# Performance work log

Hardware: AMD Instinct MI355X
Metric: run time of the kernel (lower is better)

Reference implementation:

```python
import jax, jax.numpy as jnp
import numpy as np

N_DRUG = 846
E = 64          # embedding_num
S = 1024        # neighbor_sample_size
T_LEN = 50000   # tail entity vocab
R_LEN = 100     # relation vocab
BN_EPS = 1e-5


def setup_inputs() -> dict:
    key = jax.random.key(0)
    ks = jax.random.split(key, 12)
    inp = {
        'drug_name': jnp.arange(N_DRUG, dtype=jnp.int64) if jax.config.jax_enable_x64 else jnp.arange(N_DRUG, dtype=jnp.int32),
        'adj_tail': jax.random.randint(ks[0], (N_DRUG, S), 0, T_LEN),
        'adj_relation': jax.random.randint(ks[1], (N_DRUG, S), 0, R_LEN),
        # learned parameters
        'drug_table': jax.random.normal(ks[2], (N_DRUG, E), jnp.float32),
        'rela_table': jax.random.normal(ks[3], (R_LEN, E), jnp.float32),
        'ent_table': jax.random.normal(ks[4], (T_LEN, E), jnp.float32),
        'W1': jax.random.normal(ks[5], (N_DRUG, E, E), jnp.float32),
        'b1': jax.random.normal(ks[6], (S, E), jnp.float32),
        'W2': jax.random.normal(ks[7], (N_DRUG, E, E), jnp.float32),
        'b2': jax.random.normal(ks[8], (S, E), jnp.float32),
        'lin_W': jax.random.normal(ks[9], (E, 2 * E), jnp.float32) * (6.0 / (3 * E)) ** 0.5,  # xavier-ish
        'lin_b': jnp.zeros((E,), jnp.float32),
        'bn_gamma': jnp.ones((E,), jnp.float32),
        'bn_beta': jnp.zeros((E,), jnp.float32),
    }
    return inp


def _forward(drug_table, rela_table, ent_table, W1, b1, W2, b2,
             lin_W, lin_b, bn_gamma, bn_beta,
             drug_name, adj_tail, adj_relation):
    drug_emb = drug_table[drug_name]                     # [N, E]
    rela_emb = rela_table[adj_relation]                  # [N, S, E]
    ent_emb = ent_table[adj_tail]                        # [N, S, E]

    drug_rel = drug_emb[:, None, :] * rela_emb           # [N, S, E]
    h = jax.nn.relu(jnp.einsum('nse,nef->nsf', drug_rel, W1) + b1)
    h = jnp.einsum('nse,nef->nsf', h, W2) + b2           # [N, S, E]
    score = jnp.sum(h, axis=-1)                          # [N, S]
    attn = jax.nn.softmax(score, axis=1)                 # softmax over neighbors
    weighted_ent = jnp.einsum('ns,nse->ne', attn, ent_emb)  # [N, E]

    drug_e = jnp.concatenate([weighted_ent, drug_emb], axis=1)  # [N, 2E]
    x = jax.nn.relu(drug_e @ lin_W.T + lin_b)            # [N, E]
    # BatchNorm1d in training mode: biased batch stats over the node dim
    mean = jnp.mean(x, axis=0)
    var = jnp.var(x, axis=0)
    drug_f = (x - mean) * jax.lax.rsqrt(var + BN_EPS) * bn_gamma + bn_beta
    return drug_f


def reference(drug_name, adj_tail, adj_relation, drug_table, rela_table,
              ent_table, W1, b1, W2, b2, lin_W, lin_b, bn_gamma, bn_beta):
    return _forward(drug_table, rela_table, ent_table, W1, b1, W2, b2,
                    lin_W, lin_b, bn_gamma, bn_beta,
                    drug_name, adj_tail, adj_relation)
```

## Files before the change

### kernel.cpp

```cpp
#include <hip/hip_runtime.h>

#define NDRUG 846
#define EDIM  64
#define SNB   1024
#define RLEN  100

#define XBUF_OFF  0
#define B2SUM_OFF (NDRUG*EDIM)

__global__ __launch_bounds__(256) void prep2(const float* __restrict__ b2,
                                             float* __restrict__ b2sum)
{
  int t = threadIdx.x;
  int s = blockIdx.x*64 + (t >> 2);
  int q = t & 3;
  const float4* p = reinterpret_cast<const float4*>(b2 + (size_t)s*EDIM) + q*4;
  float4 a = p[0], b = p[1], c = p[2], d = p[3];
  float v = (a.x+a.y+a.z+a.w) + (b.x+b.y+b.z+b.w)
          + (c.x+c.y+c.z+c.w) + (d.x+d.y+d.z+d.w);
  v += __shfl_xor(v, 1);
  v += __shfl_xor(v, 2);
  if (q == 0) b2sum[s] = v;
}

__global__ __launch_bounds__(512, 4) void gnn_main(
    const int*   __restrict__ adj_tail,  const int* __restrict__ adj_relation,
    const float* __restrict__ drug_table, const float* __restrict__ rela_table,
    const float* __restrict__ ent_table, const float* __restrict__ W1,
    const float* __restrict__ W2,        const float* __restrict__ b1,
    const float* __restrict__ lin_W,     const float* __restrict__ lin_b,
    const float* __restrict__ b2sum,     float* __restrict__ xbuf)
{
  __shared__ __align__(16) float lds[13128];
  float* g_s     = lds;
  float* dr_s    = lds + 6600;
  float* w2sum_s = lds + 13000;
  float* demb_s  = lds + 13064;
  float* score_s = dr_s;
  unsigned long long* msk = reinterpret_cast<unsigned long long*>(dr_s + 1024);
  float* went_s  = g_s;
  float* red_s   = g_s + 64;
  float* mred    = g_s + 576;

  int n  = blockIdx.x;
  int t  = threadIdx.x;
  int w8 = __builtin_amdgcn_readfirstlane(t >> 6);
  int ln = t & 63;

  float w1c[64];
  {
    const float* w1p = W1 + (size_t)n*4096 + ln;
    #pragma unroll
    for (int e = 0; e < 64; ++e) w1c[e] = w1p[e*64];
  }

  {
    const float4* rel4 = reinterpret_cast<const float4*>(rela_table);
    const float4* dv4  = reinterpret_cast<const float4*>(drug_table + (size_t)n*EDIM);
    float4* drw = reinterpret_cast<float4*>(dr_s);
    for (int i = t; i < 1600; i += 512) {
      float4 rv = rel4[i];
      float4 dv = dv4[i & 15];
      float4 o;
      o.x = rv.x*dv.x; o.y = rv.y*dv.y; o.z = rv.z*dv.z; o.w = rv.w*dv.w;
      drw[i] = o;
    }
    const float4* w2p4 = reinterpret_cast<const float4*>(W2 + (size_t)n*4096);
    float4 a = w2p4[t*2], b = w2p4[t*2+1];
    float s8 = (a.x+a.y+a.z+a.w) + (b.x+b.y+b.z+b.w);
    s8 += __shfl_xor(s8, 1);
    s8 += __shfl_xor(s8, 2);
    s8 += __shfl_xor(s8, 4);
    if ((t & 7) == 0) w2sum_s[t >> 3] = s8;
    if (t < EDIM) demb_s[t] = drug_table[(size_t)n*EDIM + t];
  }
  __syncthreads();

  {
    int base = (w8 < 4) ? w8*13 : 52 + (w8-4)*12;
    int nr   = (w8 < 4) ? 13 : 12;
    for (int rr = 0; rr < nr; ++rr) {
      int r = base + rr;
      const float4* drr = reinterpret_cast<const float4*>(dr_s + r*64);
      float acc = 0.f;
      #pragma unroll
      for (int e4 = 0; e4 < 16; ++e4) {
        float4 d = drr[e4];
        acc = fmaf(d.x, w1c[e4*4+0], acc);
        acc = fmaf(d.y, w1c[e4*4+1], acc);
        acc = fmaf(d.z, w1c[e4*4+2], acc);
        acc = fmaf(d.w, w1c[e4*4+3], acc);
      }
      g_s[r*66 + ln] = acc;
    }
  }
  __syncthreads();

  {
    int fq = ln & 3;
    float w2r[16];
    #pragma unroll
    for (int jj = 0; jj < 4; ++jj) {
      float4 v4 = *reinterpret_cast<const float4*>(w2sum_s + jj*16 + fq*4);
      w2r[jj*4+0] = v4.x; w2r[jj*4+1] = v4.y; w2r[jj*4+2] = v4.z; w2r[jj*4+3] = v4.w;
    }
    for (int it = 0; it < 8; ++it) {
      int s   = it*128 + (t >> 2);
      int rel = adj_relation[(size_t)n*SNB + s];
      const float4* b1r = reinterpret_cast<const float4*>(b1 + (size_t)s*EDIM);
      const float2* g2  = reinterpret_cast<const float2*>(g_s + rel*66);
      float acc = 0.f;
      #pragma unroll
      for (int jj = 0; jj < 4; ++jj) {
        float4 bv = b1r[jj*4 + fq];
        int gi = jj*8 + fq*2;
        float2 ga = g2[gi], gb = g2[gi+1];
        float h0 = fmaxf(ga.x + bv.x, 0.f);
        float h1 = fmaxf(ga.y + bv.y, 0.f);
        float h2 = fmaxf(gb.x + bv.z, 0.f);
        float h3 = fmaxf(gb.y + bv.w, 0.f);
        acc = fmaf(h0, w2r[jj*4+0], acc);
        acc = fmaf(h1, w2r[jj*4+1], acc);
        acc = fmaf(h2, w2r[jj*4+2], acc);
        acc = fmaf(h3, w2r[jj*4+3], acc);
      }
      acc += __shfl_xor(acc, 1);
      acc += __shfl_xor(acc, 2);
      if (fq == 0) score_s[s] = acc + b2sum[s];
    }
  }
  __syncthreads();

  float av0, av1;
  {
    float s0 = score_s[t], s1 = score_s[512 + t];
    float m = fmaxf(s0, s1);
    #pragma unroll
    for (int o = 32; o >= 1; o >>= 1) m = fmaxf(m, __shfl_xor(m, o));
    if (ln == 0) mred[w8] = m;
    __syncthreads();
    float M = mred[0];
    #pragma unroll
    for (int k = 1; k < 8; ++k) M = fmaxf(M, mred[k]);
    float e0 = __expf(s0 - M), e1 = __expf(s1 - M);
    float sum = e0 + e1;
    #pragma unroll
    for (int o = 32; o >= 1; o >>= 1) sum += __shfl_xor(sum, o);
    if (ln == 0) mred[8 + w8] = sum;
    __syncthreads();
    float S = mred[8];
    #pragma unroll
    for (int k = 9; k < 16; ++k) S += mred[k];
    float inv = 1.0f / S;
    av0 = e0*inv; av1 = e1*inv;
    score_s[t] = av0;
    score_s[512 + t] = av1;
  }

  {
    unsigned long long m0 = __ballot(av0 > 2e-9f);
    unsigned long long m1 = __ballot(av1 > 2e-9f);
    if (ln == 0) { msk[w8] = m0; msk[8 + w8] = m1; }
  }
  __syncthreads();
  if (w8 == 0) {
    float acc = 0.f;
    const int* tails = adj_tail + (size_t)n*SNB;
    for (int c = 0; c < 16; ++c) {
      unsigned long long mm = msk[c];
      int sbase = (c < 8) ? c*64 : 512 + (c - 8)*64;
      while (mm) {
        int bpos = __ffsll((unsigned long long)mm) - 1;
        mm &= mm - 1;
        int s = sbase + bpos;
        float av = score_s[s];
        int tl = tails[s];
        acc = fmaf(av, ent_table[(size_t)tl*EDIM + ln], acc);
      }
    }
    went_s[ln] = acc;
  }
  __syncthreads();

  {
    float acc = 0.f;
    const float* lw = lin_W + (size_t)ln*128 + w8*16;
    #pragma unroll
    for (int k = 0; k < 16; ++k) {
      int kk = w8*16 + k;
      float cv = (kk < 64) ? went_s[kk] : demb_s[kk - 64];
      acc = fmaf(cv, lw[k], acc);
    }
    red_s[w8*64 + ln] = acc;
  }
  __syncthreads();
  if (t < EDIM) {
    float x = lin_b[t];
    #pragma unroll
    for (int w = 0; w < 8; ++w) x += red_s[w*64 + t];
    xbuf[(size_t)n*EDIM + t] = fmaxf(x, 0.f);
  }
}

__global__ __launch_bounds__(256) void bn_kernel(
    const float* __restrict__ xbuf, const float* __restrict__ gamma,
    const float* __restrict__ beta, float* __restrict__ out)
{
  __shared__ float r1[4], r2[4];
  int e = blockIdx.x, t = threadIdx.x;
  float v[4];
  float s = 0.f, s2 = 0.f;
  #pragma unroll
  for (int k = 0; k < 4; ++k) {
    int nn = t + k*256;
    v[k] = (nn < NDRUG) ? xbuf[(size_t)nn*EDIM + e] : 0.f;
    s += v[k]; s2 += v[k]*v[k];
  }
  #pragma unroll
  for (int o = 32; o >= 1; o >>= 1) { s += __shfl_xor(s, o); s2 += __shfl_xor(s2, o); }
  if ((t & 63) == 0) { r1[t >> 6] = s; r2[t >> 6] = s2; }
  __syncthreads();
  float S  = r1[0] + r1[1] + r1[2] + r1[3];
  float S2 = r2[0] + r2[1] + r2[2] + r2[3];
  float mean = S / (float)NDRUG;
  float var  = S2 / (float)NDRUG - mean*mean;
  float sc   = gamma[e] * rsqrtf(var + 1e-5f);
  float sh   = beta[e] - mean*sc;
  #pragma unroll
  for (int k = 0; k < 4; ++k) {
    int nn = t + k*256;
    if (nn < NDRUG) out[(size_t)nn*EDIM + e] = v[k]*sc + sh;
  }
}

extern "C" void kernel_launch(void* const* d_in, const int* in_sizes, int n_in,
                              void* d_out, int out_size, void* d_ws, size_t ws_size,
                              hipStream_t stream)
{
  const int*   adj_tail   = (const int*)d_in[1];
  const int*   adj_rel    = (const int*)d_in[2];
  const float* drug_table = (const float*)d_in[3];
  const float* rela_table = (const float*)d_in[4];
  const float* ent_table  = (const float*)d_in[5];
  const float* W1         = (const float*)d_in[6];
  const float* b1         = (const float*)d_in[7];
  const float* W2         = (const float*)d_in[8];
  const float* b2         = (const float*)d_in[9];
  const float* lin_W      = (const float*)d_in[10];
  const float* lin_b      = (const float*)d_in[11];
  const float* gamma      = (const float*)d_in[12];
  const float* beta       = (const float*)d_in[13];

  float* ws    = (float*)d_ws;
  float* xbuf  = ws + XBUF_OFF;
  float* b2sum = ws + B2SUM_OFF;
  float* out   = (float*)d_out;

  hipLaunchKernelGGL(prep2, dim3(16), dim3(256), 0, stream, b2, b2sum);
  hipLaunchKernelGGL(gnn_main, dim3(NDRUG), dim3(512), 0, stream,
                     adj_tail, adj_rel, drug_table, rela_table, ent_table,
                     W1, W2, b1, lin_W, lin_b, b2sum, xbuf);
  hipLaunchKernelGGL(bn_kernel, dim3(EDIM), dim3(256), 0, stream,
                     xbuf, gamma, beta, out);
}
```

Before: 153.7 us.

## Compute relation-projection from global in halves and spread sparse gather across waves

The W1×(drug⊙relation) projection now folds the drug embedding into half-sized W1 register slices and reads rela_table straight from global memory. This removes the LDS staging buffer for drug⊙relation, which cuts LDS use and lets launch bounds request 8 blocks per CU instead of 4. The attention-weighted gather of entity rows is now split across all 8 waves, with weights taken by shuffle, and then reduced through LDS, where before a single wave serialised it. The cost is more global/L1 loads of rela_table per lane and an extra reduction step with a barrier.

```diff
diff --git a/kernel.cpp b/kernel.cpp
--- a/kernel.cpp
+++ b/kernel.cpp
@@ -23,7 +23,7 @@
   if (q == 0) b2sum[s] = v;
 }
 
-__global__ __launch_bounds__(512, 4) void gnn_main(
+__global__ __launch_bounds__(512, 8) void gnn_main(
     const int*   __restrict__ adj_tail,  const int* __restrict__ adj_relation,
     const float* __restrict__ drug_table, const float* __restrict__ rela_table,
     const float* __restrict__ ent_table, const float* __restrict__ W1,
@@ -31,40 +31,22 @@
     const float* __restrict__ lin_W,     const float* __restrict__ lin_b,
     const float* __restrict__ b2sum,     float* __restrict__ xbuf)
 {
-  __shared__ __align__(16) float lds[13128];
+  __shared__ __align__(16) float lds[8352];
   float* g_s     = lds;
-  float* dr_s    = lds + 6600;
-  float* w2sum_s = lds + 13000;
-  float* demb_s  = lds + 13064;
-  float* score_s = dr_s;
-  unsigned long long* msk = reinterpret_cast<unsigned long long*>(dr_s + 1024);
-  float* went_s  = g_s;
-  float* red_s   = g_s + 64;
-  float* mred    = g_s + 576;
+  float* score_s = lds + 6600;
+  float* red_s   = lds + 7624;
+  float* went_s  = lds + 8136;
+  float* demb_s  = lds + 8200;
+  float* w2sum_s = lds + 8264;
+  float* mred    = lds + 8328;
 
   int n  = blockIdx.x;
   int t  = threadIdx.x;
   int w8 = __builtin_amdgcn_readfirstlane(t >> 6);
   int ln = t & 63;
 
-  float w1c[64];
-  {
-    const float* w1p = W1 + (size_t)n*4096 + ln;
-    #pragma unroll
-    for (int e = 0; e < 64; ++e) w1c[e] = w1p[e*64];
-  }
-
-  {
-    const float4* rel4 = reinterpret_cast<const float4*>(rela_table);
-    const float4* dv4  = reinterpret_cast<const float4*>(drug_table + (size_t)n*EDIM);
-    float4* drw = reinterpret_cast<float4*>(dr_s);
-    for (int i = t; i < 1600; i += 512) {
-      float4 rv = rel4[i];
-      float4 dv = dv4[i & 15];
-      float4 o;
-      o.x = rv.x*dv.x; o.y = rv.y*dv.y; o.z = rv.z*dv.z; o.w = rv.w*dv.w;
-      drw[i] = o;
-    }
+  if (t < EDIM) demb_s[t] = drug_table[(size_t)n*EDIM + t];
+  {
     const float4* w2p4 = reinterpret_cast<const float4*>(W2 + (size_t)n*4096);
     float4 a = w2p4[t*2], b = w2p4[t*2+1];
     float s8 = (a.x+a.y+a.z+a.w) + (b.x+b.y+b.z+b.w);
@@ -72,61 +54,74 @@
     s8 += __shfl_xor(s8, 2);
     s8 += __shfl_xor(s8, 4);
     if ((t & 7) == 0) w2sum_s[t >> 3] = s8;
-    if (t < EDIM) demb_s[t] = drug_table[(size_t)n*EDIM + t];
-  }
-  __syncthreads();
-
-  {
-    int base = (w8 < 4) ? w8*13 : 52 + (w8-4)*12;
-    int nr   = (w8 < 4) ? 13 : 12;
-    for (int rr = 0; rr < nr; ++rr) {
-      int r = base + rr;
-      const float4* drr = reinterpret_cast<const float4*>(dr_s + r*64);
-      float acc = 0.f;
-      #pragma unroll
-      for (int e4 = 0; e4 < 16; ++e4) {
-        float4 d = drr[e4];
-        acc = fmaf(d.x, w1c[e4*4+0], acc);
-        acc = fmaf(d.y, w1c[e4*4+1], acc);
-        acc = fmaf(d.z, w1c[e4*4+2], acc);
-        acc = fmaf(d.w, w1c[e4*4+3], acc);
+  }
+  __syncthreads();
+
+  {
+    const float* w1p   = W1 + (size_t)n*4096 + ln;
+    const float* dembg = drug_table + (size_t)n*EDIM;
+    float acc[13];
+    int rbase = w8*13;
+    {
+      float w1c[32];
+      #pragma unroll
+      for (int e = 0; e < 32; ++e) w1c[e] = w1p[e*64] * dembg[e];
+      #pragma unroll
+      for (int rr = 0; rr < 13; ++rr) {
+        int r = rbase + rr; int rc = (r < RLEN) ? r : RLEN-1;
+        const float* rp = rela_table + (size_t)rc*EDIM;
+        float a = 0.f;
+        #pragma unroll
+        for (int e = 0; e < 32; ++e) a = fmaf(rp[e], w1c[e], a);
+        acc[rr] = a;
       }
-      g_s[r*66 + ln] = acc;
+    }
+    {
+      float w1c[32];
+      #pragma unroll
+      for (int e = 0; e < 32; ++e) w1c[e] = w1p[(e+32)*64] * dembg[e+32];
+      #pragma unroll
+      for (int rr = 0; rr < 13; ++rr) {
+        int r = rbase + rr; int rc = (r < RLEN) ? r : RLEN-1;
+        const float* rp = rela_table + (size_t)rc*EDIM + 32;
+        float a = acc[rr];
+        #pragma unroll
+        for (int e = 0; e < 32; ++e) a = fmaf(rp[e], w1c[e], a);
+        if (r < RLEN) g_s[r*66 + ln] = a;
+      }
     }
   }
   __syncthreads();
 
   {
     int fq = ln & 3;
+    int sh = t >> 2;
     float w2r[16];
     #pragma unroll
     for (int jj = 0; jj < 4; ++jj) {
       float4 v4 = *reinterpret_cast<const float4*>(w2sum_s + jj*16 + fq*4);
       w2r[jj*4+0] = v4.x; w2r[jj*4+1] = v4.y; w2r[jj*4+2] = v4.z; w2r[jj*4+3] = v4.w;
     }
+    #pragma unroll
     for (int it = 0; it < 8; ++it) {
-      int s   = it*128 + (t >> 2);
+      int s   = it*128 + sh;
       int rel = adj_relation[(size_t)n*SNB + s];
       const float4* b1r = reinterpret_cast<const float4*>(b1 + (size_t)s*EDIM);
       const float2* g2  = reinterpret_cast<const float2*>(g_s + rel*66);
-      float acc = 0.f;
+      float a2 = 0.f;
       #pragma unroll
       for (int jj = 0; jj < 4; ++jj) {
         float4 bv = b1r[jj*4 + fq];
-        int gi = jj*8 + fq*2;
-        float2 ga = g2[gi], gb = g2[gi+1];
-        float h0 = fmaxf(ga.x + bv.x, 0.f);
-        float h1 = fmaxf(ga.y + bv.y, 0.f);
-        float h2 = fmaxf(gb.x + bv.z, 0.f);
-        float h3 = fmaxf(gb.y + bv.w, 0.f);
-        acc = fmaf(h0, w2r[jj*4+0], acc);
-        acc = fmaf(h1, w2r[jj*4+1], acc);
-        acc = fmaf(h2, w2r[jj*4+2], acc);
-        acc = fmaf(h3, w2r[jj*4+3], acc);
+        float2 ga = g2[jj*8 + fq*2];
+        float2 gb = g2[jj*8 + fq*2 + 1];
+        a2 = fmaf(fmaxf(ga.x + bv.x, 0.f), w2r[jj*4+0], a2);
+        a2 = fmaf(fmaxf(ga.y + bv.y, 0.f), w2r[jj*4+1], a2);
+        a2 = fmaf(fmaxf(gb.x + bv.z, 0.f), w2r[jj*4+2], a2);
+        a2 = fmaf(fmaxf(gb.y + bv.w, 0.f), w2r[jj*4+3], a2);
       }
-      acc += __shfl_xor(acc, 1);
-      acc += __shfl_xor(acc, 2);
-      if (fq == 0) score_s[s] = acc + b2sum[s];
+      a2 += __shfl_xor(a2, 1);
+      a2 += __shfl_xor(a2, 2);
+      if (fq == 0) score_s[s] = a2 + b2sum[s];
     }
   }
   __syncthreads();
@@ -153,32 +148,33 @@
     for (int k = 9; k < 16; ++k) S += mred[k];
     float inv = 1.0f / S;
     av0 = e0*inv; av1 = e1*inv;
-    score_s[t] = av0;
-    score_s[512 + t] = av1;
   }
 
   {
     unsigned long long m0 = __ballot(av0 > 2e-9f);
     unsigned long long m1 = __ballot(av1 > 2e-9f);
-    if (ln == 0) { msk[w8] = m0; msk[8 + w8] = m1; }
-  }
-  __syncthreads();
-  if (w8 == 0) {
-    float acc = 0.f;
+    float acc4 = 0.f;
     const int* tails = adj_tail + (size_t)n*SNB;
-    for (int c = 0; c < 16; ++c) {
-      unsigned long long mm = msk[c];
-      int sbase = (c < 8) ? c*64 : 512 + (c - 8)*64;
-      while (mm) {
-        int bpos = __ffsll((unsigned long long)mm) - 1;
-        mm &= mm - 1;
-        int s = sbase + bpos;
-        float av = score_s[s];
-        int tl = tails[s];
-        acc = fmaf(av, ent_table[(size_t)tl*EDIM + ln], acc);
-      }
-    }
-    went_s[ln] = acc;
+    while (m0) {
+      int b = __ffsll(m0) - 1; m0 &= m0 - 1;
+      int s = w8*64 + b;
+      float av = __shfl(av0, b);
+      acc4 = fmaf(av, ent_table[(size_t)tails[s]*EDIM + ln], acc4);
+    }
+    while (m1) {
+      int b = __ffsll(m1) - 1; m1 &= m1 - 1;
+      int s = 512 + w8*64 + b;
+      float av = __shfl(av1, b);
+      acc4 = fmaf(av, ent_table[(size_t)tails[s]*EDIM + ln], acc4);
+    }
+    red_s[w8*64 + ln] = acc4;
+  }
+  __syncthreads();
+  if (t < EDIM) {
+    float w = red_s[t];
+    #pragma unroll
+    for (int k = 1; k < 8; ++k) w += red_s[k*64 + t];
+    went_s[t] = w;
   }
   __syncthreads();
 
```

Result: slower. 183.9 us (+19.7%).
